# Optimization experiments

Measured on AMD Instinct MI355X. Metric: run time of the kernel, lower is better.

## Reference

```python
import jax, jax.numpy as jnp
import numpy as np

T = 8192      # sequence length (scan steps)
D_IN = 1024   # input feature dim
H = 1024      # d_model (hidden size)


def setup_inputs() -> dict:
    key = jax.random.key(0)
    k1, k2, k3, k4 = jax.random.split(key, 4)
    inputs = jax.random.normal(k1, (T, D_IN), dtype=jnp.float32)
    terminations = jax.random.randint(k2, (T,), 0, 2) > 0  # bool [T]
    last_state = jnp.zeros((H,), dtype=jnp.float32)
    # GRUCell params (flax layout: input kernel with bias for all 3 gates;
    # recurrent kernel, bias only on the candidate 'n' gate).
    # Gate order within the 3H axis: [r, z, n].
    Wi = jax.random.normal(k3, (D_IN, 3 * H), dtype=jnp.float32) / np.sqrt(D_IN)
    bi = jnp.zeros((3 * H,), dtype=jnp.float32)
    Wh = jax.random.normal(k4, (H, 3 * H), dtype=jnp.float32) / np.sqrt(H)
    bhn = jnp.zeros((H,), dtype=jnp.float32)
    return {"inputs": inputs, "terminations": terminations, "last_state": last_state,
            "Wi": Wi, "bi": bi, "Wh": Wh, "bhn": bhn}


def reference(inputs, terminations, last_state, Wi, bi, Wh, bhn):
    # Precompute all input-side gate preactivations in one big GEMM: [T, 3H]
    gi_all = inputs @ Wi + bi

    def step(h, xs):
        gi, term = xs
        # reset_on_terminate: zero the carry when the episode terminated
        h = jnp.where(term, jnp.zeros_like(h), h)
        gh = h @ Wh                      # [3H], recurrent preactivations
        gi_r, gi_z, gi_n = jnp.split(gi, 3)
        gh_r, gh_z, gh_n = jnp.split(gh, 3)
        r = jax.nn.sigmoid(gi_r + gh_r)
        z = jax.nn.sigmoid(gi_z + gh_z)
        n = jnp.tanh(gi_n + r * (gh_n + bhn))
        h_new = (1.0 - z) * n + z * h    # flax GRUCell update
        # GRUout emits (new_c, (new_c, new_h)); flax GRUCell returns new_h twice
        return h_new, (h_new, h_new)

    _, (new_states, y_t) = jax.lax.scan(step, last_state, (gi_all, terminations))
    return (y_t, new_states)  # each [T, H]
```

## Files before the change

### kernel.cpp

```cpp
#include <hip/hip_runtime.h>
#include <stdint.h>

#define T_LEN 8192
#define DIN   1024
#define HD    1024
#define TH    3072
#define NB    16

typedef __attribute__((ext_vector_type(8))) short bf16x8;
typedef __attribute__((ext_vector_type(4))) float f32x4;

__device__ __forceinline__ unsigned short f2bf(float x) {
    union { float f; unsigned u; } v; v.f = x;
    unsigned r = v.u + 0x7FFFu + ((v.u >> 16) & 1u);
    return (unsigned short)(r >> 16);
}

__device__ __forceinline__ void gld16(const void* g, void* l) {
    __builtin_amdgcn_global_load_lds(
        (const __attribute__((address_space(1))) unsigned int*)(uintptr_t)g,
        (__attribute__((address_space(3))) unsigned int*)(uintptr_t)l,
        16, 0, 0);
}

__device__ __forceinline__ float sigm(float x) { return 1.f / (1.f + __expf(-x)); }
__device__ __forceinline__ float tanh_fast(float x) { return 1.f - 2.f / (1.f + __expf(2.f * x)); }

__global__ void cast_x(const float* __restrict__ X, unsigned short* __restrict__ Xb) {
    int idx = (blockIdx.x * 256 + threadIdx.x) * 4;
    float4 v = *(const float4*)(X + idx);
    ushort4 o; o.x = f2bf(v.x); o.y = f2bf(v.y); o.z = f2bf(v.z); o.w = f2bf(v.w);
    *(ushort4*)(Xb + idx) = o;
}

__global__ void transpose_cast(const float* __restrict__ Wi, const float* __restrict__ Wh,
                               unsigned short* __restrict__ WiT, unsigned short* __restrict__ WhT) {
    const float* src = blockIdx.z ? Wh : Wi;
    unsigned short* dst = blockIdx.z ? WhT : WiT;
    int n0 = blockIdx.x * 64, k0 = blockIdx.y * 64;
    __shared__ unsigned short tile[64][65];
    int tid = threadIdx.x;
    for (int p = 0; p < 16; p++) {
        int idx = tid + p * 256;
        int kl = idx >> 6, nl = idx & 63;
        tile[kl][nl] = f2bf(src[(size_t)(k0 + kl) * TH + n0 + nl]);
    }
    __syncthreads();
    for (int p = 0; p < 16; p++) {
        int idx = tid + p * 256;
        int nl = idx >> 6, kl = idx & 63;
        dst[(size_t)(n0 + nl) * 1024 + k0 + kl] = tile[kl][nl];
    }
}

__global__ void meta_kernel(const int* __restrict__ term, const float* __restrict__ last_state,
                            int* __restrict__ pos_list, int* __restrict__ meta) {
    __shared__ int part[1024];
    __shared__ int cnt[NB];
    __shared__ int cur[NB];
    __shared__ int flag;
    int tid = threadIdx.x;
    if (tid < NB) cnt[tid] = 0;
    if (tid == 0) flag = 0;
    __syncthreads();
    int base = tid * 8;
    int mx = -1;
    for (int u = 0; u < 8; u++) {
        int t = base + u;
        int s = (t == 0 || term[t] != 0) ? t : -1;
        mx = s > mx ? s : mx;
    }
    part[tid] = mx;
    __syncthreads();
    for (int d = 1; d < 1024; d <<= 1) {
        int a = part[tid];
        int b = (tid >= d) ? part[tid - d] : -1;
        __syncthreads();
        part[tid] = a > b ? a : b;
        __syncthreads();
    }
    int run = (tid > 0) ? part[tid - 1] : -1;
    int kk[8];
    for (int u = 0; u < 8; u++) {
        int t = base + u;
        int s = (t == 0 || term[t] != 0) ? t : -1;
        run = s > run ? s : run;
        int ls = t - run;
        int k = ls < NB ? ls : NB - 1;
        kk[u] = k;
        atomicAdd(&cnt[k], 1);
    }
    if (last_state[tid] != 0.0f) atomicOr(&flag, 1);
    __syncthreads();
    if (tid == 0) {
        int off = 0;
        for (int k = 0; k < NB; k++) {
            meta[k] = cnt[k];
            meta[NB + k] = off;
            cur[k] = off;
            off += cnt[k];
        }
        meta[2 * NB] = flag;
    }
    __syncthreads();
    for (int u = 0; u < 8; u++) {
        int idx = atomicAdd(&cur[kk[u]], 1);
        pos_list[idx] = base + u;
    }
}

__global__ __launch_bounds__(256) void gemm_gi(const unsigned short* __restrict__ Xb,
                                               const unsigned short* __restrict__ WiT,
                                               const float* __restrict__ bi,
                                               float* __restrict__ gi) {
    __shared__ unsigned short As[128 * 32];
    __shared__ unsigned short Bs[128 * 32];
    int tid = threadIdx.x;
    int m0 = blockIdx.y * 128, n0 = blockIdx.x * 128;
    int lane = tid & 63, wave = tid >> 6;
    int wm = wave & 1, wn = wave >> 1;
    int quad = lane >> 4, l16 = lane & 15;
    f32x4 acc[4][4] = {};
    for (int kb = 0; kb < 32; kb++) {
        int k0 = kb * 32;
        for (int p = 0; p < 2; p++) {
            int c = tid + p * 256;
            int row = c >> 2, cb = c & 3;
            gld16(Xb + (size_t)(m0 + row) * 1024 + k0 + cb * 8, As + c * 8);
            gld16(WiT + (size_t)(n0 + row) * 1024 + k0 + cb * 8, Bs + c * 8);
        }
        __syncthreads();
        bf16x8 af[4], bfr[4];
        for (int i = 0; i < 4; i++)
            af[i] = *(const bf16x8*)(As + (wm * 64 + i * 16 + l16) * 32 + quad * 8);
        for (int j = 0; j < 4; j++)
            bfr[j] = *(const bf16x8*)(Bs + (wn * 64 + j * 16 + l16) * 32 + quad * 8);
        for (int i = 0; i < 4; i++)
            for (int j = 0; j < 4; j++)
                acc[i][j] = __builtin_amdgcn_mfma_f32_16x16x32_bf16(af[i], bfr[j], acc[i][j], 0, 0, 0);
        __syncthreads();
    }
    for (int j = 0; j < 4; j++) {
        int col = n0 + wn * 64 + j * 16 + l16;
        float bv = bi[col];
        for (int i = 0; i < 4; i++) {
            int rbase = m0 + wm * 64 + i * 16 + quad * 4;
            for (int r = 0; r < 4; r++)
                gi[(size_t)(rbase + r) * TH + col] = acc[i][j][r] + bv;
        }
    }
}

__global__ void pass0_kernel(const float* __restrict__ gi, const float* __restrict__ bhn,
                             const float* __restrict__ last_state, const float* __restrict__ Wh,
                             const int* __restrict__ term, const int* __restrict__ pos_list,
                             const int* __restrict__ meta, float* __restrict__ out,
                             unsigned short* __restrict__ hb) {
    int S0 = meta[0];
    int b = blockIdx.x;
    if (b >= S0) return;
    int t = pos_list[meta[NB] + b];
    int tid = threadIdx.x;
    bool ls_path = (t == 0) && (term[0] == 0) && (meta[2 * NB] != 0);
    for (int u = 0; u < 4; u++) {
        int j = tid + u * 256;
        float gr = gi[(size_t)t * TH + j];
        float gz = gi[(size_t)t * TH + 1024 + j];
        float gn = gi[(size_t)t * TH + 2048 + j];
        float hp = 0.f, ghr = 0.f, ghz = 0.f, ghn = 0.f;
        if (ls_path) {
            hp = last_state[j];
            for (int k = 0; k < 1024; k++) {
                float hk = last_state[k];
                const float* w = Wh + (size_t)k * TH;
                ghr += hk * w[j]; ghz += hk * w[1024 + j]; ghn += hk * w[2048 + j];
            }
        }
        float r = sigm(gr + ghr);
        float z = sigm(gz + ghz);
        float n = tanh_fast(gn + r * (ghn + bhn[j]));
        float h = (1.f - z) * n + z * hp;
        out[(size_t)t * HD + j] = h;
        out[(size_t)(T_LEN + t) * HD + j] = h;
        hb[(size_t)t * HD + j] = f2bf(h);
    }
}

__global__ __launch_bounds__(256) void pass_gemm(const float* __restrict__ gi,
                                                 const float* __restrict__ bhn,
                                                 const unsigned short* __restrict__ WhT,
                                                 const unsigned short* __restrict__ hb,
                                                 float* __restrict__ out,
                                                 unsigned short* __restrict__ hbw,
                                                 const int* __restrict__ pos_list,
                                                 const int* __restrict__ meta, int k) {
    int S = meta[k];
    int r0 = blockIdx.y * 64;
    if (r0 >= S) return;
    int off = meta[NB + k];
    int j0 = blockIdx.x * 64;
    __shared__ unsigned short As[4 * 64 * 32];
    __shared__ unsigned short Bs[4 * 192 * 32];
    int tid = threadIdx.x;
    int lane = tid & 63, wave = tid >> 6;
    int wm = wave & 1, wn = wave >> 1;
    int quad = lane >> 4, l16 = lane & 15;

    int arow = tid >> 2, sub = tid & 3;
    bool av = (r0 + arow) < S;
    int t_a = av ? pos_list[off + r0 + arow] : 1;
    const unsigned short* hsrc = hb + (size_t)(t_a - 1) * HD + sub * 8;

    f32x4 acc[2][6] = {};
    for (int kb = 0; kb < 8; kb++) {
        int k0 = kb * 128;
        for (int ks = 0; ks < 4; ks++) {
            int kk0 = k0 + ks * 32;
            for (int p = 0; p < 3; p++) {
                int c = tid + p * 256;
                int row = c >> 2, q = c & 3;
                int g = row >> 6, jj = row & 63;
                gld16(WhT + (size_t)(g * 1024 + j0 + jj) * 1024 + kk0 + q * 8,
                      Bs + ks * 6144 + c * 8);
            }
            gld16(hsrc + kk0, As + ks * 2048 + tid * 8);
        }
        __syncthreads();
        for (int ks = 0; ks < 4; ks++) {
            bf16x8 af[2];
            for (int i = 0; i < 2; i++)
                af[i] = *(const bf16x8*)(As + ks * 2048 + (wm * 32 + i * 16 + l16) * 32 + quad * 8);
            for (int n = 0; n < 6; n++) {
                int g = n >> 1, jh = n & 1;
                bf16x8 bv = *(const bf16x8*)(Bs + ks * 6144 + (g * 64 + wn * 32 + jh * 16 + l16) * 32 + quad * 8);
                for (int i = 0; i < 2; i++)
                    acc[i][n] = __builtin_amdgcn_mfma_f32_16x16x32_bf16(af[i], bv, acc[i][n], 0, 0, 0);
            }
        }
        __syncthreads();
    }
    for (int i = 0; i < 2; i++) {
        for (int r = 0; r < 4; r++) {
            int rr = r0 + wm * 32 + i * 16 + quad * 4 + r;
            if (rr >= S) continue;
            int t = pos_list[off + rr];
            const float* girow = gi + (size_t)t * TH;
            const float* hprow = out + (size_t)(t - 1) * HD;
            float* o1 = out + (size_t)t * HD;
            float* o2 = out + (size_t)(T_LEN + t) * HD;
            unsigned short* hbrow = hbw + (size_t)t * HD;
            for (int jh = 0; jh < 2; jh++) {
                int j = j0 + wn * 32 + jh * 16 + l16;
                float ghr = acc[i][0 + jh][r];
                float ghz = acc[i][2 + jh][r];
                float ghn = acc[i][4 + jh][r];
                float rg = sigm(girow[j] + ghr);
                float zg = sigm(girow[1024 + j] + ghz);
                float ng = tanh_fast(girow[2048 + j] + rg * (ghn + bhn[j]));
                float h = (1.f - zg) * ng + zg * hprow[j];
                o1[j] = h;
                o2[j] = h;
                hbrow[j] = f2bf(h);
            }
        }
    }
}

__global__ void tail_kernel(const float* __restrict__ gi, const float* __restrict__ bhn,
                            const float* __restrict__ Wh,
                            const int* __restrict__ pos_list, const int* __restrict__ meta,
                            float* __restrict__ out) {
    __shared__ int pos[T_LEN];
    int S = meta[NB - 1];
    if (S == 0) return;
    int off = meta[NB + NB - 1];
    int tid = threadIdx.x;
    for (int i = tid; i < S; i += 256) pos[i] = pos_list[off + i];
    __syncthreads();
    if (tid == 0) {
        for (int i = 1; i < S; i++) {
            int v = pos[i], j = i - 1;
            while (j >= 0 && pos[j] > v) { pos[j + 1] = pos[j]; j--; }
            pos[j + 1] = v;
        }
    }
    __syncthreads();
    for (int s = 0; s < S; s++) {
        int t = pos[s];
        const float* hp = out + (size_t)(t - 1) * HD;
        const float* girow = gi + (size_t)t * TH;
        float hv[4];
        for (int c = 0; c < 4; c++) {
            int j = tid * 4 + c;
            float ghr = 0.f, ghz = 0.f, ghn = 0.f;
            for (int kk = 0; kk < 1024; kk++) {
                float hk = hp[kk];
                const float* w = Wh + (size_t)kk * TH;
                ghr += hk * w[j]; ghz += hk * w[1024 + j]; ghn += hk * w[2048 + j];
            }
            float rg = sigm(girow[j] + ghr);
            float zg = sigm(girow[1024 + j] + ghz);
            float ng = tanh_fast(girow[2048 + j] + rg * (ghn + bhn[j]));
            hv[c] = (1.f - zg) * ng + zg * hp[j];
        }
        __syncthreads();
        for (int c = 0; c < 4; c++) {
            int j = tid * 4 + c;
            out[(size_t)t * HD + j] = hv[c];
            out[(size_t)(T_LEN + t) * HD + j] = hv[c];
        }
        __syncthreads();
    }
}

extern "C" void kernel_launch(void* const* d_in, const int* in_sizes, int n_in,
                              void* d_out, int out_size, void* d_ws, size_t ws_size,
                              hipStream_t stream) {
    const float* X          = (const float*)d_in[0];
    const int*   term       = (const int*)d_in[1];
    const float* last_state = (const float*)d_in[2];
    const float* Wi         = (const float*)d_in[3];
    const float* bi         = (const float*)d_in[4];
    const float* Wh         = (const float*)d_in[5];
    const float* bhn        = (const float*)d_in[6];
    float* out = (float*)d_out;

    char* ws = (char*)d_ws;
    float*          gi       = (float*)ws;
    unsigned short* Xb       = (unsigned short*)(ws + 100663296);
    unsigned short* hb       = Xb;
    unsigned short* WiT      = (unsigned short*)(ws + 117440512);
    unsigned short* WhT      = (unsigned short*)(ws + 123731968);
    int*            pos_list = (int*)(ws + 130023424);
    int*            meta     = (int*)(ws + 130056192);

    cast_x<<<dim3(8192), dim3(256), 0, stream>>>(X, Xb);
    transpose_cast<<<dim3(48, 16, 2), dim3(256), 0, stream>>>(Wi, Wh, WiT, WhT);
    meta_kernel<<<dim3(1), dim3(1024), 0, stream>>>(term, last_state, pos_list, meta);
    gemm_gi<<<dim3(24, 64), dim3(256), 0, stream>>>(Xb, WiT, bi, gi);
    pass0_kernel<<<dim3(8192), dim3(256), 0, stream>>>(gi, bhn, last_state, Wh, term, pos_list, meta, out, hb);
    for (int k = 1; k < NB - 1; k++) {
        int rows_max = T_LEN / (k + 1);
        int gy = (rows_max + 63) / 64;
        pass_gemm<<<dim3(16, gy), dim3(256), 0, stream>>>(gi, bhn, WhT, hb, out, hb, pos_list, meta, k);
    }
    tail_kernel<<<dim3(1), dim3(256), 0, stream>>>(gi, bhn, Wh, pos_list, meta, out);
}
```

Baseline: 439.1 us.

## Fuse per-depth recurrence launches into one persistent cooperative kernel with LDS-resident Wh

Replaces the 14 separate pass_gemm launches with one cooperative persistent kernel of 256 blocks. Each block permanently caches a 16-column slice of the bf16 recurrent weights for all three gates in shared memory (96 KB), so Wh is not reloaded from global memory on every pass. Waves stream A rows directly from global memory and a grid-wide sync separates the depth levels. The aim is to remove launch overhead and repeated weight traffic, at the cost of grid-sync latency, reduced occupancy from the large LDS footprint, and uncached global A loads.

```diff
diff --git a/kernel.cpp b/kernel.cpp
--- a/kernel.cpp
+++ b/kernel.cpp
@@ -1,4 +1,5 @@
 #include <hip/hip_runtime.h>
+#include <hip/hip_cooperative_groups.h>
 #include <stdint.h>
 
 #define T_LEN 8192
@@ -6,6 +7,8 @@
 #define HD    1024
 #define TH    3072
 #define NB    16
+
+namespace coop = cooperative_groups;
 
 typedef __attribute__((ext_vector_type(8))) short bf16x8;
 typedef __attribute__((ext_vector_type(4))) float f32x4;
@@ -186,83 +189,77 @@
     }
 }
 
-__global__ __launch_bounds__(256) void pass_gemm(const float* __restrict__ gi,
-                                                 const float* __restrict__ bhn,
-                                                 const unsigned short* __restrict__ WhT,
-                                                 const unsigned short* __restrict__ hb,
-                                                 float* __restrict__ out,
-                                                 unsigned short* __restrict__ hbw,
-                                                 const int* __restrict__ pos_list,
-                                                 const int* __restrict__ meta, int k) {
-    int S = meta[k];
-    int r0 = blockIdx.y * 64;
-    if (r0 >= S) return;
-    int off = meta[NB + k];
-    int j0 = blockIdx.x * 64;
-    __shared__ unsigned short As[4 * 64 * 32];
-    __shared__ unsigned short Bs[4 * 192 * 32];
-    int tid = threadIdx.x;
+__global__ __launch_bounds__(512, 2) void recur_all(
+        const float* __restrict__ gi, const float* __restrict__ bhn,
+        const unsigned short* __restrict__ WhT, unsigned short* __restrict__ hb,
+        float* __restrict__ out, const int* __restrict__ pos_list,
+        const int* __restrict__ meta) {
+    __shared__ unsigned short Bs[49152];
+    int tid = threadIdx.x;
+    int cg = blockIdx.x & 63;
+    int rg = blockIdx.x >> 6;
+    int j0 = cg * 16;
     int lane = tid & 63, wave = tid >> 6;
-    int wm = wave & 1, wn = wave >> 1;
-    int quad = lane >> 4, l16 = lane & 15;
-
-    int arow = tid >> 2, sub = tid & 3;
-    bool av = (r0 + arow) < S;
-    int t_a = av ? pos_list[off + r0 + arow] : 1;
-    const unsigned short* hsrc = hb + (size_t)(t_a - 1) * HD + sub * 8;
-
-    f32x4 acc[2][6] = {};
-    for (int kb = 0; kb < 8; kb++) {
-        int k0 = kb * 128;
-        for (int ks = 0; ks < 4; ks++) {
-            int kk0 = k0 + ks * 32;
-            for (int p = 0; p < 3; p++) {
-                int c = tid + p * 256;
-                int row = c >> 2, q = c & 3;
-                int g = row >> 6, jj = row & 63;
-                gld16(WhT + (size_t)(g * 1024 + j0 + jj) * 1024 + kk0 + q * 8,
-                      Bs + ks * 6144 + c * 8);
+    int l16 = lane & 15, quad = lane >> 4;
+    int worker = rg * 8 + wave;
+
+    for (int p = 0; p < 12; p++) {
+        int c = tid + p * 512;
+        int col = c & 15, q = (c >> 4) & 3, ks = (c >> 6) & 31, g = c >> 11;
+        gld16(WhT + (size_t)(g * 1024 + j0 + col) * 1024 + ks * 32 + q * 8,
+              Bs + (size_t)c * 8);
+    }
+    __syncthreads();
+
+    coop::grid_group grid = coop::this_grid();
+
+    for (int k = 1; k <= NB - 2; k++) {
+        int S = meta[k];
+        if (S == 0) break;
+        int off = meta[NB + k];
+        for (int i = worker; i * 32 < S; i += 32) {
+            int r0 = i * 32;
+            int ra0 = r0 + l16;      ra0 = ra0 < S ? ra0 : S - 1;
+            int ra1 = r0 + 16 + l16; ra1 = ra1 < S ? ra1 : S - 1;
+            int t0 = pos_list[off + ra0];
+            int t1 = pos_list[off + ra1];
+            const unsigned short* ap0 = hb + (size_t)(t0 - 1) * HD + quad * 8;
+            const unsigned short* ap1 = hb + (size_t)(t1 - 1) * HD + quad * 8;
+            f32x4 acc[2][3] = {};
+            #pragma unroll
+            for (int ks = 0; ks < 32; ks++) {
+                bf16x8 a0 = *(const bf16x8*)(ap0 + ks * 32);
+                bf16x8 a1 = *(const bf16x8*)(ap1 + ks * 32);
+                #pragma unroll
+                for (int g = 0; g < 3; g++) {
+                    bf16x8 bv = *(const bf16x8*)(Bs + ((size_t)((g * 32 + ks) * 4 + quad) * 16 + l16) * 8);
+                    acc[0][g] = __builtin_amdgcn_mfma_f32_16x16x32_bf16(a0, bv, acc[0][g], 0, 0, 0);
+                    acc[1][g] = __builtin_amdgcn_mfma_f32_16x16x32_bf16(a1, bv, acc[1][g], 0, 0, 0);
+                }
             }
-            gld16(hsrc + kk0, As + ks * 2048 + tid * 8);
-        }
-        __syncthreads();
-        for (int ks = 0; ks < 4; ks++) {
-            bf16x8 af[2];
-            for (int i = 0; i < 2; i++)
-                af[i] = *(const bf16x8*)(As + ks * 2048 + (wm * 32 + i * 16 + l16) * 32 + quad * 8);
-            for (int n = 0; n < 6; n++) {
-                int g = n >> 1, jh = n & 1;
-                bf16x8 bv = *(const bf16x8*)(Bs + ks * 6144 + (g * 64 + wn * 32 + jh * 16 + l16) * 32 + quad * 8);
-                for (int i = 0; i < 2; i++)
-                    acc[i][n] = __builtin_amdgcn_mfma_f32_16x16x32_bf16(af[i], bv, acc[i][n], 0, 0, 0);
+            #pragma unroll
+            for (int h2 = 0; h2 < 2; h2++) {
+                #pragma unroll
+                for (int r = 0; r < 4; r++) {
+                    int rr = r0 + h2 * 16 + quad * 4 + r;
+                    if (rr >= S) continue;
+                    int t = pos_list[off + rr];
+                    int j = j0 + l16;
+                    float ghr = acc[h2][0][r], ghz = acc[h2][1][r], ghn = acc[h2][2][r];
+                    const float* girow = gi + (size_t)t * TH;
+                    float hp = out[(size_t)(t - 1) * HD + j];
+                    float rgt = sigm(girow[j] + ghr);
+                    float zgt = sigm(girow[1024 + j] + ghz);
+                    float ngt = tanh_fast(girow[2048 + j] + rgt * (ghn + bhn[j]));
+                    float hv = (1.f - zgt) * ngt + zgt * hp;
+                    out[(size_t)t * HD + j] = hv;
+                    out[(size_t)(T_LEN + t) * HD + j] = hv;
+                    hb[(size_t)t * HD + j] = f2bf(hv);
+                }
             }
         }
-        __syncthreads();
-    }
-    for (int i = 0; i < 2; i++) {
-        for (int r = 0; r < 4; r++) {
-            int rr = r0 + wm * 32 + i * 16 + quad * 4 + r;
-            if (rr >= S) continue;
-            int t = pos_list[off + rr];
-            const float* girow = gi + (size_t)t * TH;
-            const float* hprow = out + (size_t)(t - 1) * HD;
-            float* o1 = out + (size_t)t * HD;
-            float* o2 = out + (size_t)(T_LEN + t) * HD;
-            unsigned short* hbrow = hbw + (size_t)t * HD;
-            for (int jh = 0; jh < 2; jh++) {
-                int j = j0 + wn * 32 + jh * 16 + l16;
-                float ghr = acc[i][0 + jh][r];
-                float ghz = acc[i][2 + jh][r];
-                float ghn = acc[i][4 + jh][r];
-                float rg = sigm(girow[j] + ghr);
-                float zg = sigm(girow[1024 + j] + ghz);
-                float ng = tanh_fast(girow[2048 + j] + rg * (ghn + bhn[j]));
-                float h = (1.f - zg) * ng + zg * hprow[j];
-                o1[j] = h;
-                o2[j] = h;
-                hbrow[j] = f2bf(h);
-            }
-        }
+        __threadfence();
+        grid.sync();
     }
 }
 
@@ -339,10 +336,13 @@
     meta_kernel<<<dim3(1), dim3(1024), 0, stream>>>(term, last_state, pos_list, meta);
     gemm_gi<<<dim3(24, 64), dim3(256), 0, stream>>>(Xb, WiT, bi, gi);
     pass0_kernel<<<dim3(8192), dim3(256), 0, stream>>>(gi, bhn, last_state, Wh, term, pos_list, meta, out, hb);
-    for (int k = 1; k < NB - 1; k++) {
-        int rows_max = T_LEN / (k + 1);
-        int gy = (rows_max + 63) / 64;
-        pass_gemm<<<dim3(16, gy), dim3(256), 0, stream>>>(gi, bhn, WhT, hb, out, hb, pos_list, meta, k);
-    }
+
+    {
+        void* args[] = { (void*)&gi, (void*)&bhn, (void*)&WhT, (void*)&hb,
+                         (void*)&out, (void*)&pos_list, (void*)&meta };
+        hipLaunchCooperativeKernel((void*)recur_all, dim3(256), dim3(512),
+                                   args, 0, stream);
+    }
+
     tail_kernel<<<dim3(1), dim3(256), 0, stream>>>(gi, bhn, Wh, pos_list, meta, out);
 }
```

Result: slower. 1.427 ms (+225.0%).
